# Performance work log

Measured on AMD Instinct MI355X. Metric: run time of the kernel, lower is better.

## Reference

```python
import jax, jax.numpy as jnp
import numpy as np

K_CENTERS = 128   # SA K
RADIUS = 1.0      # SA r
D = 3             # spatial dim (module-level d)
IFD = 64          # input feature dim
L1, L2, L3 = 64, 64, 128
N_POINTS = 8192


def setup_inputs() -> dict:
    key = jax.random.key(0)
    ks = jax.random.split(key, 8)
    coords = jax.random.normal(ks[0], (N_POINTS, D), dtype=jnp.float32)
    features = jax.random.normal(ks[1], (N_POINTS, IFD), dtype=jnp.float32)

    def lin(kw, kb, fan_in, fan_out):
        bound = 1.0 / np.sqrt(fan_in)
        W = jax.random.uniform(kw, (fan_in, fan_out), jnp.float32, -bound, bound)
        b = jax.random.uniform(kb, (fan_out,), jnp.float32, -bound, bound)
        return W, b

    W1, b1 = lin(ks[2], ks[3], D + IFD, L1)
    W2, b2 = lin(ks[4], ks[5], L1, L2)
    W3, b3 = lin(ks[6], ks[7], L2, L3)
    return dict(coords=coords, features=features,
                W1=W1, b1=b1, W2=W2, b2=b2, W3=W3, b3=b3)


def farthest_point_sample(coords, k):
    """Iterative FPS starting from point 0 (pytorch3d default). Returns [k] indices."""
    n = coords.shape[0]

    def step(carry, _):
        dists, last = carry
        d2 = jnp.sum((coords - coords[last]) ** 2, axis=1)  # [N]
        dists = jnp.minimum(dists, d2)
        nxt = jnp.argmax(dists).astype(jnp.int32)
        return (dists, nxt), nxt

    init = (jnp.full((n,), 1e10, coords.dtype), jnp.int32(0))
    (_, _), rest = jax.lax.scan(step, init, None, length=k - 1)
    return jnp.concatenate([jnp.zeros((1,), jnp.int32), rest])


def reference(coords, features, W1, b1, W2, b2, W3, b3):
    # 1) Farthest point sampling -> K centers
    idx = farthest_point_sample(coords, K_CENTERS)
    centers = coords[idx]                                  # [K, 3]

    # 2) Ball-query grouping (mask form): point p in group(c) iff ||p - c|| < r.
    rel = coords[None, :, :] - centers[:, None, :]         # [K, N, 3] (coords - center)
    mask = jnp.linalg.norm(rel, axis=-1) < RADIUS          # [K, N]

    # 3) Per-group PointNet: shared MLP on [rel_coords, features], then masked max over group.
    feat = jnp.broadcast_to(features[None, :, :], (K_CENTERS,) + features.shape)
    x = jnp.concatenate([rel, feat], axis=-1)              # [K, N, 3+ifd]
    h = jax.nn.relu(x @ W1 + b1)                           # [K, N, l1]
    h = jax.nn.relu(h @ W2 + b2)                           # [K, N, l2]
    h = jax.nn.relu(h @ W3 + b3)                           # [K, N, l3]
    h = jnp.where(mask[..., None], h, -jnp.inf)            # exclude out-of-ball points
    out_features = jnp.max(h, axis=1)                      # [K, l3]
    return centers, out_features
```

## Files before the change

### kernel.cpp

```cpp
#include <hip/hip_runtime.h>

#define NPTS 8192
#define KC   128
#define IFD  64
#define DL1  64
#define DL2  64
#define DL3  128
#define SPLITS 8
#define PPB  (NPTS/SPLITS)
#define NTASK (KC*SPLITS)
#define FPT  16

__global__ __launch_bounds__(256) void f1_kernel(const float* __restrict__ features,
                                                 const float* __restrict__ W1,
                                                 const float* __restrict__ b1,
                                                 float* __restrict__ F1) {
    const int tid = threadIdx.x;
    const int d = tid & 63;
    const int p = (int)blockIdx.x * 4 + (tid >> 6);
    float acc = b1[d];
    const float* frow = features + p * IFD;
#pragma unroll 8
    for (int a = 0; a < IFD; ++a) {
        acc += frow[a] * W1[(3 + a) * DL1 + d];
    }
    F1[p * DL1 + d] = acc;
}

__global__ __attribute__((amdgpu_flat_work_group_size(512, 512),
                          amdgpu_waves_per_eu(2, 2)))
void fused_kernel(const float* __restrict__ coords,
                  const float* __restrict__ F1,
                  const float* __restrict__ W1,
                  const float* __restrict__ W2,
                  const float* __restrict__ b2,
                  const float* __restrict__ W3,
                  const float* __restrict__ b3,
                  float* centers,
                  float* __restrict__ outf) {
    __shared__ float sW1r[3 * 64];
    __shared__ float sb2[64];
    __shared__ float sb3[128];
    __shared__ unsigned short list[PPB];
    __shared__ int cnt;
    __shared__ float scc[3];
    __shared__ float h1[64 * 65];
    __shared__ float h2T[64 * 68];
    __shared__ float red[16 * 128];
    __shared__ float wv[2][8];
    __shared__ int   widx[2];

    const int tid = threadIdx.x;

    if (blockIdx.x == 0) {
        {
#pragma clang fp contract(off)
            float px[FPT], py[FPT], pz[FPT], dist[FPT];
#pragma unroll
            for (int i = 0; i < FPT; ++i) {
                const int n = i * 512 + tid;
                px[i] = coords[n * 3 + 0];
                py[i] = coords[n * 3 + 1];
                pz[i] = coords[n * 3 + 2];
                dist[i] = 1e10f;
            }
            if (tid == 0) { widx[0] = 0x7FFFFFFF; widx[1] = 0x7FFFFFFF; }

            float cx = coords[0], cy = coords[1], cz = coords[2];
            if (tid == 0) {
                atomicExch(&centers[0], cx);
                atomicExch(&centers[1], cy);
                atomicExch(&centers[2], cz);
            }
            __syncthreads();

            for (int s = 1; s < KC; ++s) {
                const int buf = s & 1;
                float bv = -1.0f;
#pragma unroll
                for (int i = 0; i < FPT; ++i) {
                    const float dx = px[i] - cx;
                    const float dy = py[i] - cy;
                    const float dz = pz[i] - cz;
                    const float t2 = (dx * dx + dy * dy) + dz * dz;
                    const float dm = dist[i] < t2 ? dist[i] : t2;
                    dist[i] = dm;
                    bv = fmaxf(bv, dm);
                }
#pragma unroll
                for (int off = 32; off > 0; off >>= 1) {
                    bv = fmaxf(bv, __shfl_down(bv, off));
                }
                if ((tid & 63) == 0) wv[buf][tid >> 6] = bv;
                __syncthreads();
                float gv = wv[buf][0];
#pragma unroll
                for (int w = 1; w < 8; ++w) gv = fmaxf(gv, wv[buf][w]);
                int ln = 0x7FFFFFFF;
#pragma unroll
                for (int i = 0; i < FPT; ++i) {
                    if (dist[i] == gv) ln = min(ln, i * 512 + tid);
                }
                if (ln != 0x7FFFFFFF) atomicMin(&widx[buf], ln);
                __syncthreads();
                const int w = widx[buf];
                if (tid == 0) widx[buf ^ 1] = 0x7FFFFFFF;
                cx = coords[w * 3 + 0];
                cy = coords[w * 3 + 1];
                cz = coords[w * 3 + 2];
                if (tid == 0) {
                    atomicExch(&centers[s * 3 + 0], cx);
                    atomicExch(&centers[s * 3 + 1], cy);
                    atomicExch(&centers[s * 3 + 2], cz);
                }
            }
        }
        return;
    }

    if (tid < 192) sW1r[tid] = W1[tid];
    if (tid < 64)  sb2[tid] = b2[tid];
    if (tid < 128) sb3[tid] = b3[tid];
    __syncthreads();

    for (int k = 0;; ++k) {
        const int t = (int)(blockIdx.x - 1) + 255 * k;
        if (t >= NTASK) break;
        const int c = t >> 3;
        const int base = (t & 7) * PPB;

        if (tid == 0) {
            float x, y, z;
            for (;;) {
                x = atomicAdd(&centers[c * 3 + 0], 0.0f);
                y = atomicAdd(&centers[c * 3 + 1], 0.0f);
                z = atomicAdd(&centers[c * 3 + 2], 0.0f);
                if (x != 0.0f && y != 0.0f && z != 0.0f) break;
                __builtin_amdgcn_s_sleep(8);
            }
            scc[0] = x; scc[1] = y; scc[2] = z; cnt = 0;
        }
        __syncthreads();
        const float cx = scc[0], cy = scc[1], cz = scc[2];

        {
#pragma clang fp contract(off)
            for (int j = tid; j < PPB; j += 512) {
                const int n = base + j;
                const float dx = coords[n * 3 + 0] - cx;
                const float dy = coords[n * 3 + 1] - cy;
                const float dz = coords[n * 3 + 2] - cz;
                const float d2 = (dx * dx + dy * dy) + dz * dz;
                if (sqrtf(d2) < 1.0f) {
                    const int pos = atomicAdd(&cnt, 1);
                    list[pos] = (unsigned short)n;
                }
            }
        }
        __syncthreads();
        const int count = cnt;
        if (count > 0) {
            float rmax[4] = {0.f, 0.f, 0.f, 0.f};
            const int ntiles = (count + 63) >> 6;
            for (int T = 0; T < ntiles; ++T) {
                {
                    const int d = tid & 63;
                    const int pr = tid >> 6;
#pragma unroll
                    for (int r = 0; r < 8; ++r) {
                        const int p = r * 8 + pr;
                        const int li = T * 64 + p;
                        const int n = (li < count) ? (int)list[li] : (int)list[0];
                        const float rx = coords[n * 3 + 0] - cx;
                        const float ry = coords[n * 3 + 1] - cy;
                        const float rz = coords[n * 3 + 2] - cz;
                        float v = F1[n * DL1 + d];
                        v += rx * sW1r[d] + ry * sW1r[64 + d] + rz * sW1r[128 + d];
                        h1[p * 65 + d] = v > 0.f ? v : 0.f;
                    }
                }
                __syncthreads();
                {
                    const int p0 = (tid & 31) * 2;
                    const int d0 = (tid >> 5) * 4;
                    float acc[2][4];
#pragma unroll
                    for (int a = 0; a < 2; ++a)
#pragma unroll
                        for (int j = 0; j < 4; ++j) acc[a][j] = sb2[d0 + j];
                    for (int i = 0; i < 64; ++i) {
                        const float h0 = h1[p0 * 65 + i];
                        const float hA = h1[(p0 + 1) * 65 + i];
                        const float4 w = *reinterpret_cast<const float4*>(&W2[i * DL2 + d0]);
                        acc[0][0] += h0 * w.x; acc[0][1] += h0 * w.y;
                        acc[0][2] += h0 * w.z; acc[0][3] += h0 * w.w;
                        acc[1][0] += hA * w.x; acc[1][1] += hA * w.y;
                        acc[1][2] += hA * w.z; acc[1][3] += hA * w.w;
                    }
#pragma unroll
                    for (int j = 0; j < 4; ++j) {
                        h2T[(d0 + j) * 68 + p0]     = fmaxf(acc[0][j], 0.f);
                        h2T[(d0 + j) * 68 + p0 + 1] = fmaxf(acc[1][j], 0.f);
                    }
                }
                __syncthreads();
                {
                    const int p0 = (tid >> 5) * 4;
                    const int d0 = (tid & 31) * 4;
                    float acc[4][4];
#pragma unroll
                    for (int p = 0; p < 4; ++p)
#pragma unroll
                        for (int j = 0; j < 4; ++j) acc[p][j] = sb3[d0 + j];
                    for (int i = 0; i < 64; ++i) {
                        const float4 hv = *reinterpret_cast<const float4*>(&h2T[i * 68 + p0]);
                        const float4 w = *reinterpret_cast<const float4*>(&W3[i * DL3 + d0]);
                        const float hh[4] = {hv.x, hv.y, hv.z, hv.w};
#pragma unroll
                        for (int p = 0; p < 4; ++p) {
                            acc[p][0] += hh[p] * w.x;
                            acc[p][1] += hh[p] * w.y;
                            acc[p][2] += hh[p] * w.z;
                            acc[p][3] += hh[p] * w.w;
                        }
                    }
#pragma unroll
                    for (int j = 0; j < 4; ++j) {
                        float m = acc[0][j];
#pragma unroll
                        for (int p = 1; p < 4; ++p) m = fmaxf(m, acc[p][j]);
                        m = fmaxf(m, 0.f);
                        rmax[j] = fmaxf(rmax[j], m);
                    }
                }
                __syncthreads();
            }
            {
                const int pg = tid >> 5;
                const int d0 = (tid & 31) * 4;
#pragma unroll
                for (int j = 0; j < 4; ++j) red[pg * 128 + d0 + j] = rmax[j];
            }
            __syncthreads();
            if (tid < 128) {
                float m = red[tid];
#pragma unroll
                for (int pg = 1; pg < 16; ++pg) m = fmaxf(m, red[pg * 128 + tid]);
                atomicMax((int*)&outf[c * 128 + tid], __float_as_int(m));
            }
        }
    }
}

extern "C" void kernel_launch(void* const* d_in, const int* in_sizes, int n_in,
                              void* d_out, int out_size, void* d_ws, size_t ws_size,
                              hipStream_t stream) {
    (void)in_sizes; (void)n_in; (void)ws_size;
    const float* coords   = (const float*)d_in[0];
    const float* features = (const float*)d_in[1];
    const float* W1 = (const float*)d_in[2];
    const float* b1 = (const float*)d_in[3];
    const float* W2 = (const float*)d_in[4];
    const float* b2 = (const float*)d_in[5];
    const float* W3 = (const float*)d_in[6];
    const float* b3 = (const float*)d_in[7];
    float* out = (float*)d_out;
    float* F1  = (float*)d_ws;

    (void)hipMemsetAsync(d_out, 0, (size_t)out_size * sizeof(float), stream);

    f1_kernel<<<NPTS / 4, 256, 0, stream>>>(features, W1, b1, F1);
    fused_kernel<<<256, 512, 0, stream>>>(coords, F1, W1, W2, b2, W3, b3,
                                          out, out + KC * 3);
}
```

Before: 237.2 us.

## Fuse F1 precompute into consumer blocks and streamline FPS argmax reduction

Removes the separate F1 kernel. The 255 consumer blocks now compute F1 rows and zero the output features while block 0 runs FPS, and they sync through a global counter before first use. The FPS loop now carries the argmax index through the shuffle and shared-memory reduction, replacing a second pass with atomicMin and one barrier. This overlaps the F1 GEMV with the serial FPS critical path and trims per-iteration sync, at the cost of relying on co-residency of all blocks for the spin-wait.

```diff
diff --git a/kernel.cpp b/kernel.cpp
--- a/kernel.cpp
+++ b/kernel.cpp
@@ -10,34 +10,22 @@
 #define PPB  (NPTS/SPLITS)
 #define NTASK (KC*SPLITS)
 #define FPT  16
-
-__global__ __launch_bounds__(256) void f1_kernel(const float* __restrict__ features,
-                                                 const float* __restrict__ W1,
-                                                 const float* __restrict__ b1,
-                                                 float* __restrict__ F1) {
-    const int tid = threadIdx.x;
-    const int d = tid & 63;
-    const int p = (int)blockIdx.x * 4 + (tid >> 6);
-    float acc = b1[d];
-    const float* frow = features + p * IFD;
-#pragma unroll 8
-    for (int a = 0; a < IFD; ++a) {
-        acc += frow[a] * W1[(3 + a) * DL1 + d];
-    }
-    F1[p * DL1 + d] = acc;
-}
+#define NCONS 255
 
 __global__ __attribute__((amdgpu_flat_work_group_size(512, 512),
                           amdgpu_waves_per_eu(2, 2)))
 void fused_kernel(const float* __restrict__ coords,
-                  const float* __restrict__ F1,
+                  const float* __restrict__ features,
                   const float* __restrict__ W1,
+                  const float* __restrict__ b1,
                   const float* __restrict__ W2,
                   const float* __restrict__ b2,
                   const float* __restrict__ W3,
                   const float* __restrict__ b3,
                   float* centers,
-                  float* __restrict__ outf) {
+                  float* __restrict__ outf,
+                  float* __restrict__ F1,
+                  int*   f1ctr) {
     __shared__ float sW1r[3 * 64];
     __shared__ float sb2[64];
     __shared__ float sb3[128];
@@ -47,12 +35,13 @@
     __shared__ float h1[64 * 65];
     __shared__ float h2T[64 * 68];
     __shared__ float red[16 * 128];
-    __shared__ float wv[2][8];
-    __shared__ int   widx[2];
+    __shared__ float wvv[2][8];
+    __shared__ int   wvi[2][8];
 
     const int tid = threadIdx.x;
-
-    if (blockIdx.x == 0) {
+    const int b   = (int)blockIdx.x;
+
+    if (b == 0) {
         {
 #pragma clang fp contract(off)
             float px[FPT], py[FPT], pz[FPT], dist[FPT];
@@ -64,19 +53,17 @@
                 pz[i] = coords[n * 3 + 2];
                 dist[i] = 1e10f;
             }
-            if (tid == 0) { widx[0] = 0x7FFFFFFF; widx[1] = 0x7FFFFFFF; }
-
             float cx = coords[0], cy = coords[1], cz = coords[2];
             if (tid == 0) {
                 atomicExch(&centers[0], cx);
                 atomicExch(&centers[1], cy);
                 atomicExch(&centers[2], cz);
             }
-            __syncthreads();
 
             for (int s = 1; s < KC; ++s) {
                 const int buf = s & 1;
                 float bv = -1.0f;
+                int   bi = 0;
 #pragma unroll
                 for (int i = 0; i < FPT; ++i) {
                     const float dx = px[i] - cx;
@@ -85,26 +72,34 @@
                     const float t2 = (dx * dx + dy * dy) + dz * dz;
                     const float dm = dist[i] < t2 ? dist[i] : t2;
                     dist[i] = dm;
-                    bv = fmaxf(bv, dm);
+                    const bool win = dm > bv;
+                    bv = win ? dm : bv;
+                    bi = win ? i * 512 + tid : bi;
                 }
 #pragma unroll
                 for (int off = 32; off > 0; off >>= 1) {
-                    bv = fmaxf(bv, __shfl_down(bv, off));
-                }
-                if ((tid & 63) == 0) wv[buf][tid >> 6] = bv;
-                __syncthreads();
-                float gv = wv[buf][0];
-#pragma unroll
-                for (int w = 1; w < 8; ++w) gv = fmaxf(gv, wv[buf][w]);
-                int ln = 0x7FFFFFFF;
-#pragma unroll
-                for (int i = 0; i < FPT; ++i) {
-                    if (dist[i] == gv) ln = min(ln, i * 512 + tid);
-                }
-                if (ln != 0x7FFFFFFF) atomicMin(&widx[buf], ln);
-                __syncthreads();
-                const int w = widx[buf];
-                if (tid == 0) widx[buf ^ 1] = 0x7FFFFFFF;
+                    const float ov = __shfl_down(bv, off);
+                    const int   oi = __shfl_down(bi, off);
+                    const bool take = (ov > bv) || (ov == bv && oi < bi);
+                    bv = take ? ov : bv;
+                    bi = take ? oi : bi;
+                }
+                if ((tid & 63) == 0) {
+                    wvv[buf][tid >> 6] = bv;
+                    wvi[buf][tid >> 6] = bi;
+                }
+                __syncthreads();
+                float gv = wvv[buf][0];
+                int   gi = wvi[buf][0];
+#pragma unroll
+                for (int w = 1; w < 8; ++w) {
+                    const float v = wvv[buf][w];
+                    const int   i = wvi[buf][w];
+                    const bool take = (v > gv) || (v == gv && i < gi);
+                    gv = take ? v : gv;
+                    gi = take ? i : gi;
+                }
+                const int w = __builtin_amdgcn_readfirstlane(gi);
                 cx = coords[w * 3 + 0];
                 cy = coords[w * 3 + 1];
                 cz = coords[w * 3 + 2];
@@ -118,13 +113,37 @@
         return;
     }
 
+    {
+        const int z0 = (b - 1) * 65;
+        if (tid < 65 && z0 + tid < KC * DL3) outf[z0 + tid] = 0.0f;
+        const int d = tid & 63;
+#pragma unroll
+        for (int j = 0; j < 5; ++j) {
+            const int rloc = j * 8 + (tid >> 6);
+            const int r = (b - 1) + NCONS * rloc;
+            if (r < NPTS) {
+                float acc = b1[d];
+                const float* frow = features + r * IFD;
+#pragma unroll 8
+                for (int a = 0; a < IFD; ++a) {
+                    acc += frow[a] * W1[(3 + a) * DL1 + d];
+                }
+                F1[r * DL1 + d] = acc;
+            }
+        }
+        __threadfence();
+        __syncthreads();
+        if (tid == 0) atomicAdd(f1ctr, 1);
+    }
+
     if (tid < 192) sW1r[tid] = W1[tid];
     if (tid < 64)  sb2[tid] = b2[tid];
     if (tid < 128) sb3[tid] = b3[tid];
     __syncthreads();
 
+    bool f1_ready = false;
     for (int k = 0;; ++k) {
-        const int t = (int)(blockIdx.x - 1) + 255 * k;
+        const int t = (b - 1) + NCONS * k;
         if (t >= NTASK) break;
         const int c = t >> 3;
         const int base = (t & 7) * PPB;
@@ -136,7 +155,7 @@
                 y = atomicAdd(&centers[c * 3 + 1], 0.0f);
                 z = atomicAdd(&centers[c * 3 + 2], 0.0f);
                 if (x != 0.0f && y != 0.0f && z != 0.0f) break;
-                __builtin_amdgcn_s_sleep(8);
+                __builtin_amdgcn_s_sleep(2);
             }
             scc[0] = x; scc[1] = y; scc[2] = z; cnt = 0;
         }
@@ -159,7 +178,15 @@
         }
         __syncthreads();
         const int count = cnt;
+
         if (count > 0) {
+            if (!f1_ready) {
+                if (tid == 0) {
+                    while (atomicAdd(f1ctr, 0) < NCONS) __builtin_amdgcn_s_sleep(2);
+                }
+                __syncthreads();
+                f1_ready = true;
+            }
             float rmax[4] = {0.f, 0.f, 0.f, 0.f};
             const int ntiles = (count + 63) >> 6;
             for (int T = 0; T < ntiles; ++T) {
@@ -255,7 +282,7 @@
 extern "C" void kernel_launch(void* const* d_in, const int* in_sizes, int n_in,
                               void* d_out, int out_size, void* d_ws, size_t ws_size,
                               hipStream_t stream) {
-    (void)in_sizes; (void)n_in; (void)ws_size;
+    (void)in_sizes; (void)n_in; (void)ws_size; (void)out_size;
     const float* coords   = (const float*)d_in[0];
     const float* features = (const float*)d_in[1];
     const float* W1 = (const float*)d_in[2];
@@ -265,11 +292,12 @@
     const float* W3 = (const float*)d_in[6];
     const float* b3 = (const float*)d_in[7];
     float* out = (float*)d_out;
-    float* F1  = (float*)d_ws;
-
-    (void)hipMemsetAsync(d_out, 0, (size_t)out_size * sizeof(float), stream);
-
-    f1_kernel<<<NPTS / 4, 256, 0, stream>>>(features, W1, b1, F1);
-    fused_kernel<<<256, 512, 0, stream>>>(coords, F1, W1, W2, b2, W3, b3,
-                                          out, out + KC * 3);
+    int*   f1ctr = (int*)d_ws;
+    float* F1    = (float*)d_ws + 16;
+
+    (void)hipMemsetAsync(d_out, 0, KC * 3 * sizeof(float), stream);
+    (void)hipMemsetAsync(d_ws, 0, sizeof(int), stream);
+
+    fused_kernel<<<256, 512, 0, stream>>>(coords, features, W1, b1, W2, b2, W3, b3,
+                                          out, out + KC * 3, F1, f1ctr);
 }
```

Result: slower. 293.2 us (+23.6%).
